# Optimization experiments

Hardware: AMD Instinct MI355X
Metric: run time of the kernel (lower is better)

Reference implementation:

```python
import jax, jax.numpy as jnp
import numpy as np
from jax import lax

BS = 8  # block size
NF = 64  # num_feat

def _dct_mat(n=BS):
    k = np.arange(n)
    D = np.cos(np.pi * (2 * k[None, :] + 1) * k[:, None] / (2 * n)) * np.sqrt(2.0 / n)
    D[0] = np.sqrt(1.0 / n)
    return jnp.asarray(D, dtype=jnp.float32)  # orthonormal DCT-II basis [8,8]

D_DCT = _dct_mat()

def conv2d(x, w, b, stride=1, padding=0, dilation=1, groups=1):
    out = lax.conv_general_dilated(
        x, w, window_strides=(stride, stride),
        padding=[(padding, padding), (padding, padding)],
        rhs_dilation=(dilation, dilation),
        feature_group_count=groups,
        dimension_numbers=('NCHW', 'OIHW', 'NCHW'))
    return out + b[None, :, None, None]

def block_dct_idct(x, bs=BS):
    # fused per-8x8-block DDCT followed by IDDCT (orthonormal basis ->
    # mathematically identity, computed explicitly as in the original loop)
    B, C, H, W = x.shape
    xb = x.reshape(B, C, H // bs, bs, W // bs, bs)
    CB = jnp.einsum('ij,bchjwk,lk->bchiwl', D_DCT, xb, D_DCT)   # D X D^T
    out = jnp.einsum('ji,bchjwk,kl->bchiwl', D_DCT, CB, D_DCT)  # D^T Y D
    return out.reshape(B, C, H, W)

def setup_inputs() -> dict:
    key = jax.random.key(0)
    ks = jax.random.split(key, 16)
    s = 0.05
    inp = {
        'x': jax.random.normal(ks[0], (2, 72, 256, 256), dtype=jnp.float32),
        'conv_w': jax.random.normal(ks[1], (64, 72, 3, 3), dtype=jnp.float32) * s,
        'conv_b': jnp.zeros((64,), dtype=jnp.float32),
        # 7 distinct directional_dct_layer instances (branch 6 reuses layer 4's weights, as in the source)
        'ddct_w': jax.random.normal(ks[2], (7, 64, 64, 3, 3), dtype=jnp.float32) * s,
        'ddct_b': jnp.zeros((7, 64), dtype=jnp.float32),
        'dctc_w': jax.random.normal(ks[3], (7, 64, 1, 3, 3), dtype=jnp.float32) * s,  # groups=64 depthwise
        'dctc_b': jnp.zeros((7, 64), dtype=jnp.float32),
        'dw1_w': jax.random.normal(ks[4], (32, 72, 3, 3), dtype=jnp.float32) * s,
        'dw1_b': jnp.zeros((32,), dtype=jnp.float32),
        'dw3_w': jax.random.normal(ks[5], (512, 32, 1, 1), dtype=jnp.float32) * s,
        'dw3_b': jnp.zeros((512,), dtype=jnp.float32),
        'ar_w': jax.random.normal(ks[6], (72, 512, 3, 3), dtype=jnp.float32) * s,
        'ar_b': jnp.zeros((72,), dtype=jnp.float32),
    }
    return inp

def reference(x, conv_w, conv_b, ddct_w, ddct_b, dctc_w, dctc_b,
              dw1_w, dw1_b, dw3_w, dw3_b, ar_w, ar_b):
    B, _, H, W = x.shape
    feat = jax.nn.gelu(conv2d(x, conv_w, conv_b, padding=1), approximate=False)
    # branches use layers [0,1,3,4,5,6(->4),7,8]; branch 6 reuses conv_dct_4
    layer_idx = [0, 1, 2, 3, 4, 3, 5, 6]
    outs = []
    for li in layer_idx:
        y = jax.nn.gelu(conv2d(feat, ddct_w[li], ddct_b[li], padding=1), approximate=False) + feat
        y = conv2d(y, dctc_w[li], dctc_b[li], stride=8, padding=2, dilation=2, groups=NF)
        y = block_dct_idct(y)
        y = jax.image.resize(y, (B, NF, H, W), method='bilinear')  # align_corners=False
        outs.append(y)
    w = jax.nn.sigmoid(conv2d(jax.nn.relu(conv2d(x, dw1_w, dw1_b, padding=1)), dw3_w, dw3_b, padding=0))
    gated = jnp.concatenate([o * w[:, i * NF:(i + 1) * NF] for i, o in enumerate(outs)], axis=1)
    return conv2d(gated, ar_w, ar_b, padding=1)
```

## Files before the change

kernel.cpp:

```cpp
#include <hip/hip_runtime.h>
#include <hip/hip_bf16.h>

#define BB 2
#define HH 256
#define WW 256
#define HW (HH*WW)
#define GP 258
#define GPP (GP*GP)

typedef __attribute__((ext_vector_type(8))) short bf16x8;
typedef __attribute__((ext_vector_type(4))) float f32x4;

__device__ __forceinline__ float geluf(float x) {
    return 0.5f * x * (1.0f + erff(x * 0.7071067811865475f));
}

__device__ __forceinline__ ushort f2bf(float f) {
    __hip_bfloat16 h = __float2bfloat16(f);
    return *reinterpret_cast<ushort*>(&h);
}
__device__ __forceinline__ float bf2f(ushort u) {
    uint v = ((uint)u) << 16;
    return *reinterpret_cast<float*>(&v);
}

__device__ __forceinline__ int dec96(int i) {
    int q = i / 3, r = i - q * 3;
    return q * 8 + (r == 0 ? 0 : (r == 1 ? 2 : 6));
}

__global__ __launch_bounds__(256) void xpose_kernel(
    const float* __restrict__ x, ushort* __restrict__ xt)
{
    const int pix = blockIdx.x * 256 + threadIdx.x;
    const int b   = pix >> 16;
    const int rem = pix & 65535;

    uint w[48];
    const float* xb = x + (size_t)b * 72 * HW + rem;
    #pragma unroll
    for (int i = 0; i < 36; ++i) {
        const ushort lo = f2bf(xb[(size_t)(2 * i)     * HW]);
        const ushort hi = f2bf(xb[(size_t)(2 * i + 1) * HW]);
        w[i] = (uint)lo | ((uint)hi << 16);
    }
    #pragma unroll
    for (int i = 36; i < 48; ++i) w[i] = 0;

    uint* dst = reinterpret_cast<uint*>(xt + (size_t)pix * 96);
    #pragma unroll
    for (int k = 0; k < 12; ++k) {
        uint4 u = { w[4*k], w[4*k+1], w[4*k+2], w[4*k+3] };
        *reinterpret_cast<uint4*>(dst + 4 * k) = u;
    }
}

__global__ __launch_bounds__(256) void prepack_w1_kernel(
    const float* __restrict__ conv_w, const float* __restrict__ dw1_w,
    ushort* __restrict__ wpc1)
{
    const int idx = blockIdx.x * 256 + threadIdx.x;
    if (idx >= 9 * 3 * 6 * 64) return;
    const int lane = idx & 63;
    int rest = idx >> 6;
    const int mf = rest % 6; rest /= 6;
    const int cb = rest % 3;
    const int t  = rest / 3;
    const int co  = mf * 16 + (lane & 15);
    const int ci0 = cb * 32 + (lane >> 4) * 8;
    ushort* dst = wpc1 + (size_t)idx * 8;
    #pragma unroll
    for (int j = 0; j < 8; ++j) {
        const int ci = ci0 + j;
        float w = 0.0f;
        if (ci < 72)
            w = (co < 64) ? conv_w[((size_t)co * 72 + ci) * 9 + t]
                          : dw1_w[((size_t)(co - 64) * 72 + ci) * 9 + t];
        dst[j] = f2bf(w);
    }
}

__global__ __launch_bounds__(256) void conv1dw1_mfma_kernel(
    const ushort* __restrict__ xt, const ushort* __restrict__ wpc1,
    const float* __restrict__ conv_b, const float* __restrict__ dw1_b,
    ushort* __restrict__ fg, float* __restrict__ relu1)
{
    const int lane = threadIdx.x & 63;
    const int wave = threadIdx.x >> 6;
    const int l15  = lane & 15;
    const int lg   = lane >> 4;

    const int bid  = blockIdx.x;
    const int b    = bid >> 9;
    const int rest = bid & 511;
    const int y    = rest >> 1;
    const int x0   = (rest & 1) * 128 + wave * 32;

    f32x4 acc[6][2];
    #pragma unroll
    for (int mf = 0; mf < 6; ++mf)
        #pragma unroll
        for (int nf = 0; nf < 2; ++nf)
            acc[mf][nf] = (f32x4){0.f, 0.f, 0.f, 0.f};

    const bf16x8 zero8 = {};

    #pragma unroll 1
    for (int t = 0; t < 9; ++t) {
        const int dy = t / 3 - 1, dx = t % 3 - 1;
        const int yy = y + dy;
        if ((unsigned)yy >= (unsigned)HH) continue;

        const int xA = x0 + l15 + dx;
        const int xB = xA + 16;
        const bool va = (unsigned)xA < (unsigned)WW;
        const bool vb = (unsigned)xB < (unsigned)WW;
        const int xAc = min(max(xA, 0), WW - 1);
        const int xBc = min(xB, WW - 1);

        const ushort* rowbase = xt + ((size_t)(b * HH + yy) * WW) * 96;
        const ushort* pA = rowbase + (size_t)xAc * 96 + lg * 8;
        const ushort* pB = rowbase + (size_t)xBc * 96 + lg * 8;
        const ushort* wp = wpc1 + (size_t)(t * 3) * (6 * 512) + lane * 8;

        #pragma unroll
        for (int cb = 0; cb < 3; ++cb) {
            bf16x8 B0 = *reinterpret_cast<const bf16x8*>(pA + cb * 32);
            bf16x8 B1 = *reinterpret_cast<const bf16x8*>(pB + cb * 32);
            B0 = va ? B0 : zero8;
            B1 = vb ? B1 : zero8;
            const ushort* wpc = wp + (size_t)cb * (6 * 512);
            #pragma unroll
            for (int mf = 0; mf < 6; ++mf) {
                const bf16x8 A = *reinterpret_cast<const bf16x8*>(wpc + mf * 512);
                acc[mf][0] = __builtin_amdgcn_mfma_f32_16x16x32_bf16(A, B0, acc[mf][0], 0, 0, 0);
                acc[mf][1] = __builtin_amdgcn_mfma_f32_16x16x32_bf16(A, B1, acc[mf][1], 0, 0, 0);
            }
        }
    }

    #pragma unroll
    for (int nf = 0; nf < 2; ++nf) {
        const int xx = x0 + nf * 16 + l15;
        ushort* fgp = fg + ((size_t)(b * HH + y) * WW + xx) * 64;
        #pragma unroll
        for (int mf = 0; mf < 4; ++mf) {
            const int co = mf * 16 + lg * 4;
            ushort pk[4];
            #pragma unroll
            for (int r = 0; r < 4; ++r)
                pk[r] = f2bf(geluf(acc[mf][nf][r] + conv_b[co + r]));
            *reinterpret_cast<uint2*>(fgp + co) = *reinterpret_cast<uint2*>(pk);
        }
    }
    #pragma unroll
    for (int mf = 4; mf < 6; ++mf) {
        const int co = (mf - 4) * 16 + lg * 4;
        #pragma unroll
        for (int nf = 0; nf < 2; ++nf) {
            const int xx = x0 + nf * 16 + l15;
            float* op = relu1 + ((size_t)(b * 32 + co) * HH + y) * WW + xx;
            #pragma unroll
            for (int r = 0; r < 4; ++r)
                op[(size_t)r * HW] = fmaxf(acc[mf][nf][r] + dw1_b[co + r], 0.0f);
        }
    }
}

__global__ __launch_bounds__(256) void prepack_wb_kernel(
    const float* __restrict__ ddct_w, ushort* __restrict__ wpb)
{
    const int idx = blockIdx.x * 256 + threadIdx.x;
    if (idx >= 7 * 9 * 2 * 4 * 64) return;
    const int lane = idx & 63;
    int rest = idx >> 6;
    const int mf = rest & 3; rest >>= 2;
    const int cb = rest & 1; rest >>= 1;
    const int t  = rest % 9;
    const int li = rest / 9;
    const int co  = mf * 16 + (lane & 15);
    const int ci0 = cb * 32 + (lane >> 4) * 8;
    ushort* dst = wpb + (size_t)idx * 8;
    #pragma unroll
    for (int j = 0; j < 8; ++j)
        dst[j] = f2bf(ddct_w[(((size_t)li * 64 + co) * 64 + ci0 + j) * 9 + t]);
}

__global__ __launch_bounds__(256) void branch_mfma_kernel(
    const ushort* __restrict__ fg, const ushort* __restrict__ wpb,
    const float* __restrict__ ddct_b, float* __restrict__ ycomp)
{
    const int lane = threadIdx.x & 63;
    const int wave = threadIdx.x >> 6;
    const int l15  = lane & 15;
    const int lg   = lane >> 4;

    int bid = blockIdx.x;
    const int t72 = bid % 72; bid /= 72;
    const int b  = bid & 1;
    const int li = bid >> 1;
    const int widx = t72 * 4 + wave;
    const int r  = widx / 3;
    const int c0 = (widx - r * 3) * 32;
    const int R  = dec96(r);

    const int cA = c0 + l15, cB = cA + 16;
    const int CA = dec96(cA), CB2 = dec96(cB);

    f32x4 acc[4][2];
    #pragma unroll
    for (int mf = 0; mf < 4; ++mf)
        #pragma unroll
        for (int nf = 0; nf < 2; ++nf)
            acc[mf][nf] = (f32x4){0.f, 0.f, 0.f, 0.f};

    const bf16x8 zero8 = {};
    const ushort* fgb = fg + (size_t)b * HW * 64;

    #pragma unroll 1
    for (int t = 0; t < 9; ++t) {
        const int dy = t / 3 - 1, dx = t % 3 - 1;
        const int yy = R + dy;
        if ((unsigned)yy >= (unsigned)HH) continue;

        const int xA = CA + dx, xB = CB2 + dx;
        const bool va = (unsigned)xA < (unsigned)WW;
        const bool vb = (unsigned)xB < (unsigned)WW;
        const int xAc = min(max(xA, 0), WW - 1);
        const int xBc = min(max(xB, 0), WW - 1);

        const ushort* rowb = fgb + (size_t)yy * WW * 64;
        const ushort* pA = rowb + (size_t)xAc * 64 + lg * 8;
        const ushort* pB = rowb + (size_t)xBc * 64 + lg * 8;
        const ushort* wp = wpb + (size_t)((li * 9 + t) * 2) * (4 * 512) + lane * 8;

        #pragma unroll
        for (int cb = 0; cb < 2; ++cb) {
            bf16x8 B0 = *reinterpret_cast<const bf16x8*>(pA + cb * 32);
            bf16x8 B1 = *reinterpret_cast<const bf16x8*>(pB + cb * 32);
            B0 = va ? B0 : zero8;
            B1 = vb ? B1 : zero8;
            const ushort* wpc = wp + (size_t)cb * (4 * 512);
            #pragma unroll
            for (int mf = 0; mf < 4; ++mf) {
                const bf16x8 A = *reinterpret_cast<const bf16x8*>(wpc + mf * 512);
                acc[mf][0] = __builtin_amdgcn_mfma_f32_16x16x32_bf16(A, B0, acc[mf][0], 0, 0, 0);
                acc[mf][1] = __builtin_amdgcn_mfma_f32_16x16x32_bf16(A, B1, acc[mf][1], 0, 0, 0);
            }
        }
    }

    #pragma unroll
    for (int nf = 0; nf < 2; ++nf) {
        const int c = c0 + nf * 16 + l15;
        const int C = dec96(c);
        const ushort* res = fgb + ((size_t)R * WW + C) * 64;
        #pragma unroll
        for (int mf = 0; mf < 4; ++mf) {
            const int co = mf * 16 + lg * 4;
            ushort r4[4];
            *reinterpret_cast<uint2*>(r4) = *reinterpret_cast<const uint2*>(res + co);
            #pragma unroll
            for (int rr = 0; rr < 4; ++rr) {
                const float v = geluf(acc[mf][nf][rr] + ddct_b[li * 64 + co + rr]) + bf2f(r4[rr]);
                ycomp[((((size_t)li * BB + b) * 64 + co + rr) * 96 + r) * 96 + c] = v;
            }
        }
    }
}

__global__ __launch_bounds__(256) void dctc_kernel(
    const float* __restrict__ ycomp, const float* __restrict__ dctc_w,
    const float* __restrict__ dctc_b, float* __restrict__ s_all)
{
    const int idx = blockIdx.x * 256 + threadIdx.x;
    if (idx >= 7 * BB * 64 * 32 * 32) return;
    const int ow = idx & 31;
    const int oh = (idx >> 5) & 31;
    const int c  = (idx >> 10) & 63;
    const int b  = (idx >> 16) & (BB - 1);
    const int li = idx >> 17;

    const float* yc = ycomp + (((size_t)li * BB + b) * 64 + c) * (96 * 96);
    const float* w  = dctc_w + (li * 64 + c) * 9;
    float acc = dctc_b[li * 64 + c];
    #pragma unroll
    for (int ky = 0; ky < 3; ++ky) {
        const int cr = 3 * oh + ky - 1;
        if (cr < 0) continue;
        #pragma unroll
        for (int kx = 0; kx < 3; ++kx) {
            const int cc = 3 * ow + kx - 1;
            if (cc < 0) continue;
            acc = fmaf(yc[cr * 96 + cc], w[ky * 3 + kx], acc);
        }
    }
    s_all[idx] = acc;
}

__global__ __launch_bounds__(256) void prepack_w3_kernel(
    const float* __restrict__ dw3_w, float* __restrict__ dw3t)
{
    const int idx = blockIdx.x * 256 + threadIdx.x;
    if (idx >= 32 * 512) return;
    const int ch = idx & 511;
    const int k  = idx >> 9;
    dw3t[k * 512 + ch] = dw3_w[ch * 32 + k];
}

__global__ __launch_bounds__(256) void halo_zero_kernel(ushort* __restrict__ gt)
{
    const int PB = 2 * GP * 64 + 2 * 256 * 64;
    const int i = blockIdx.x * 256 + threadIdx.x;
    if (i >= BB * PB) return;
    const int b = i / PB;
    int r = i - b * PB;
    size_t px;
    int c4;
    if (r < 2 * GP * 64) {
        const int rr = r / (GP * 64);
        int rem = r - rr * (GP * 64);
        const int xp = rem / 64; c4 = rem % 64;
        px = (size_t)(rr ? GP - 1 : 0) * GP + xp;
    } else {
        r -= 2 * GP * 64;
        const int side = r / (256 * 64);
        int rem = r - side * (256 * 64);
        const int yp = 1 + rem / 64; c4 = rem % 64;
        px = (size_t)yp * GP + (side ? GP - 1 : 0);
    }
    const uint4 z = {0u, 0u, 0u, 0u};
    *reinterpret_cast<uint4*>(gt + ((size_t)b * GPP + px) * 512 + c4 * 8) = z;
}

__global__ __launch_bounds__(256, 3) void gated_nhwc_kernel(
    const float* __restrict__ relu1, const float* __restrict__ dw3t,
    const float* __restrict__ dw3_b, const float* __restrict__ s_all,
    ushort* __restrict__ gt)
{
    __shared__ float sm[32][32];
    const int pix0 = blockIdx.x * 32;
    const int b  = pix0 >> 16;
    const int y  = (pix0 >> 8) & 255;
    const int x0 = pix0 & 255;

    {
        const int spx = threadIdx.x & 31;
        const int k0  = threadIdx.x >> 5;
        const float* rbase = relu1 + (size_t)b * 32 * HW + (size_t)y * WW + x0 + spx;
        #pragma unroll
        for (int i = 0; i < 4; ++i)
            sm[k0 + 8 * i][spx] = rbase[(size_t)(k0 + 8 * i) * HW];
    }
    __syncthreads();

    const int ch0 = threadIdx.x * 2;
    const int branch = ch0 >> 6;
    const int c0 = ch0 & 63;
    const int lmap[8] = {0, 1, 2, 3, 4, 3, 5, 6};
    const int li = lmap[branch];

    const float bb0 = dw3_b[ch0], bb1 = dw3_b[ch0 + 1];

    float2 wreg[32];
    #pragma unroll
    for (int k = 0; k < 32; ++k)
        wreg[k] = *reinterpret_cast<const float2*>(dw3t + k * 512 + ch0);

    float acc0[32], acc1[32];
    #pragma unroll
    for (int px = 0; px < 32; ++px) { acc0[px] = bb0; acc1[px] = bb1; }

    #pragma unroll
    for (int k = 0; k < 32; ++k) {
        const float w0k = wreg[k].x;
        const float w1k = wreg[k].y;
        const float4* row = reinterpret_cast<const float4*>(&sm[k][0]);
        #pragma unroll
        for (int q = 0; q < 8; ++q) {
            const float4 r4 = row[q];
            acc0[q*4+0] = fmaf(r4.x, w0k, acc0[q*4+0]);
            acc0[q*4+1] = fmaf(r4.y, w0k, acc0[q*4+1]);
            acc0[q*4+2] = fmaf(r4.z, w0k, acc0[q*4+2]);
            acc0[q*4+3] = fmaf(r4.w, w0k, acc0[q*4+3]);
            acc1[q*4+0] = fmaf(r4.x, w1k, acc1[q*4+0]);
            acc1[q*4+1] = fmaf(r4.y, w1k, acc1[q*4+1]);
            acc1[q*4+2] = fmaf(r4.z, w1k, acc1[q*4+2]);
            acc1[q*4+3] = fmaf(r4.w, w1k, acc1[q*4+3]);
        }
    }

    const float* sp0 = s_all + (((size_t)li * BB + b) * 64 + c0) * 1024;
    const float* sp1 = sp0 + 1024;

    const float sy = (y + 0.5f) * 0.125f - 0.5f;
    const float fy0f = floorf(sy);
    const float fy = sy - fy0f;
    int y0 = (int)fy0f;
    const int y1 = min(y0 + 1, 31);
    y0 = max(y0, 0);

    float n0[6], n1[6];
    const int xb = (x0 >> 3) - 1;
    #pragma unroll
    for (int jj = 0; jj < 6; ++jj) {
        const int xn = min(max(xb + jj, 0), 31);
        const float a00 = sp0[y0 * 32 + xn], a01 = sp0[y1 * 32 + xn];
        const float a10 = sp1[y0 * 32 + xn], a11 = sp1[y1 * 32 + xn];
        n0[jj] = a00 + fy * (a01 - a00);
        n1[jj] = a10 + fy * (a11 - a10);
    }

    ushort* gbase = gt + (((size_t)b * GPP) + (size_t)(y + 1) * GP + (x0 + 1)) * 512 + ch0;
    #pragma unroll
    for (int px = 0; px < 32; ++px) {
        const int   j  = (px + 4) >> 3;
        const float fx = (float)((px + 4) & 7) * 0.125f + 0.0625f;
        const float va = n0[j] + fx * (n0[j + 1] - n0[j]);
        const float vb = n1[j] + fx * (n1[j + 1] - n1[j]);
        const float g0 = 1.0f / (1.0f + exp2f(-1.4426950408889634f * acc0[px]));
        const float g1 = 1.0f / (1.0f + exp2f(-1.4426950408889634f * acc1[px]));
        const uint pack = (uint)f2bf(va * g0) | ((uint)f2bf(vb * g1) << 16);
        *reinterpret_cast<uint*>(gbase + (size_t)px * 512) = pack;
    }
}

__global__ __launch_bounds__(256) void prepack_w_kernel(
    const float* __restrict__ ar_w, ushort* __restrict__ wpack)
{
    const int idx = blockIdx.x * 256 + threadIdx.x;
    if (idx >= 16 * 9 * 5 * 64) return;
    const int lane = idx & 63;
    int rest = idx >> 6;
    const int mf = rest % 5; rest /= 5;
    const int t  = rest % 9;
    const int cb = rest / 9;
    const int co  = mf * 16 + (lane & 15);
    const int ci0 = cb * 32 + (lane >> 4) * 8;
    ushort* dst = wpack + (size_t)idx * 8;
    #pragma unroll
    for (int j = 0; j < 8; ++j) {
        const float w = (co < 72) ? ar_w[((size_t)co * 512 + ci0 + j) * 9 + t] : 0.0f;
        dst[j] = f2bf(w);
    }
}

#define WPK_CHUNK (9 * 5 * 512)

__global__ __launch_bounds__(256, 2) void conv_ar_mfma_kernel(
    const ushort* __restrict__ gt, const ushort* __restrict__ wpack,
    const float* __restrict__ ar_b, float* __restrict__ out)
{
    __shared__ ushort smw[WPK_CHUNK];
    const int tid  = threadIdx.x;
    const int lane = tid & 63;
    const int wave = tid >> 6;
    const int l15  = lane & 15;
    const int lg   = lane >> 4;

    const int lb = (blockIdx.x & 7) * 64 + (blockIdx.x >> 3);
    const int b  = lb >> 8;
    const int y  = lb & 255;
    const int x0 = wave * 64;

    f32x4 acc[5][4];
    #pragma unroll
    for (int mf = 0; mf < 5; ++mf)
        #pragma unroll
        for (int nf = 0; nf < 4; ++nf)
            acc[mf][nf] = (f32x4){0.f, 0.f, 0.f, 0.f};

    const ushort* rowp[3];
    #pragma unroll
    for (int dy = 0; dy < 3; ++dy)
        rowp[dy] = gt + ((size_t)b * GPP + (size_t)(y + dy) * GP) * 512;
    int off[3][4];
    #pragma unroll
    for (int dx = 0; dx < 3; ++dx)
        #pragma unroll
        for (int nf = 0; nf < 4; ++nf)
            off[dx][nf] = (x0 + nf * 16 + l15 + dx) * 512 + lg * 8;

    uint4 streg[12];
    {
        const uint4* s = reinterpret_cast<const uint4*>(wpack);
        #pragma unroll
        for (int i = 0; i < 12; ++i) {
            const int e = i * 256 + tid;
            streg[i] = (e < 2880) ? s[e] : (uint4){0u, 0u, 0u, 0u};
        }
        uint4* d = reinterpret_cast<uint4*>(smw);
        #pragma unroll
        for (int i = 0; i < 12; ++i) {
            const int e = i * 256 + tid;
            if (e < 2880) d[e] = streg[i];
        }
    }
    __syncthreads();

    #pragma unroll 1
    for (int cb = 0; cb < 16; ++cb) {
        if (cb < 15) {
            const uint4* s = reinterpret_cast<const uint4*>(
                wpack + (size_t)(cb + 1) * WPK_CHUNK);
            #pragma unroll
            for (int i = 0; i < 12; ++i) {
                const int e = i * 256 + tid;
                if (e < 2880) streg[i] = s[e];
            }
        }

        const int cbo = cb * 32;
        bf16x8 Bcur[4], Bnxt[4];
        #pragma unroll
        for (int nf = 0; nf < 4; ++nf)
            Bcur[nf] = *reinterpret_cast<const bf16x8*>(rowp[0] + off[0][nf] + cbo);

        #pragma unroll
        for (int t = 0; t < 9; ++t) {
            if (t < 8) {
                const int dyn = (t + 1) / 3, dxn = (t + 1) % 3;
                #pragma unroll
                for (int nf = 0; nf < 4; ++nf)
                    Bnxt[nf] = *reinterpret_cast<const bf16x8*>(
                        rowp[dyn] + off[dxn][nf] + cbo);
            }
            #pragma unroll
            for (int mf = 0; mf < 5; ++mf) {
                const bf16x8 A = *reinterpret_cast<const bf16x8*>(
                    smw + (t * 5 + mf) * 512 + lane * 8);
                #pragma unroll
                for (int nf = 0; nf < 4; ++nf)
                    acc[mf][nf] = __builtin_amdgcn_mfma_f32_16x16x32_bf16(
                        A, Bcur[nf], acc[mf][nf], 0, 0, 0);
            }
            if (t < 8) {
                #pragma unroll
                for (int nf = 0; nf < 4; ++nf) Bcur[nf] = Bnxt[nf];
            }
        }

        __syncthreads();
        if (cb < 15) {
            uint4* d = reinterpret_cast<uint4*>(smw);
            #pragma unroll
            for (int i = 0; i < 12; ++i) {
                const int e = i * 256 + tid;
                if (e < 2880) d[e] = streg[i];
            }
        }
        __syncthreads();
    }

    #pragma unroll
    for (int mf = 0; mf < 5; ++mf) {
        const int co = mf * 16 + lg * 4;
        if (co >= 72) continue;
        #pragma unroll
        for (int nf = 0; nf < 4; ++nf) {
            const int x = x0 + nf * 16 + l15;
            float* op = out + (((size_t)(b * 72 + co) * HH + y) * WW) + x;
            #pragma unroll
            for (int r = 0; r < 4; ++r)
                op[(size_t)r * HW] = acc[mf][nf][r] + ar_b[co + r];
        }
    }
}

extern "C" void kernel_launch(void* const* d_in, const int* in_sizes, int n_in,
                              void* d_out, int out_size, void* d_ws, size_t ws_size,
                              hipStream_t stream) {
    const float* x      = (const float*)d_in[0];
    const float* conv_w = (const float*)d_in[1];
    const float* conv_b = (const float*)d_in[2];
    const float* ddct_w = (const float*)d_in[3];
    const float* ddct_b = (const float*)d_in[4];
    const float* dctc_w = (const float*)d_in[5];
    const float* dctc_b = (const float*)d_in[6];
    const float* dw1_w  = (const float*)d_in[7];
    const float* dw1_b  = (const float*)d_in[8];
    const float* dw3_w  = (const float*)d_in[9];
    const float* dw3_b  = (const float*)d_in[10];
    const float* ar_w   = (const float*)d_in[11];
    const float* ar_b   = (const float*)d_in[12];
    float* out = (float*)d_out;

    float* ws = (float*)d_ws;
    ushort* gated_t = (ushort*)ws;
    ushort* fg    = (ushort*)ws;
    float* ycomp  = ws + 4194304;
    float* s_all  = ws + 34080768;
    float* relu1  = ws + 34998272;
    ushort* wpack = (ushort*)(ws + 39192576);
    ushort* wpb   = (ushort*)(ws + 39376896);
    ushort* wpc1  = (ushort*)(ws + 39505920);
    ushort* xt    = (ushort*)(ws + 39547392);
    float* dw3t   = ws + 45838848;

    prepack_w_kernel<<<dim3(180), dim3(256), 0, stream>>>(ar_w, wpack);
    prepack_wb_kernel<<<dim3(126), dim3(256), 0, stream>>>(ddct_w, wpb);
    prepack_w1_kernel<<<dim3(41), dim3(256), 0, stream>>>(conv_w, dw1_w, wpc1);
    prepack_w3_kernel<<<dim3(64), dim3(256), 0, stream>>>(dw3_w, dw3t);
    xpose_kernel<<<dim3(BB * HW / 256), dim3(256), 0, stream>>>(x, xt);

    conv1dw1_mfma_kernel<<<dim3(BB * HH * 2), dim3(256), 0, stream>>>(
        xt, wpc1, conv_b, dw1_b, fg, relu1);

    branch_mfma_kernel<<<dim3(7 * BB * 72), dim3(256), 0, stream>>>(
        fg, wpb, ddct_b, ycomp);

    dctc_kernel<<<dim3((7 * BB * 64 * 32 * 32) / 256), dim3(256), 0, stream>>>(
        ycomp, dctc_w, dctc_b, s_all);

    halo_zero_kernel<<<dim3(514), dim3(256), 0, stream>>>(gated_t);

    gated_nhwc_kernel<<<dim3(BB * HW / 32), dim3(256), 0, stream>>>(
        relu1, dw3t, dw3_b, s_all, gated_t);

    conv_ar_mfma_kernel<<<dim3(BB * HH), dim3(256), 0, stream>>>(
        gated_t, wpack, ar_b, out);
}
```

Measured before the change: 396.1 us.

## Read AR conv weights directly from global and halve per-wave tile for occupancy

The final 512->72 3x3 conv kernel drops its shared-memory weight staging and barrier-synchronised double buffering. Each lane now loads its MFMA A fragments straight from the prepacked global weight buffer, relying on L1/L2 caching. The per-wave output tile shrinks from 64 to 32 pixels, the grid doubles, and launch bounds rise to 4 blocks per CU to raise occupancy. The B prefetch also now carries across channel blocks. The cost is more global and cache traffic for weights and less weight reuse per load.

```diff
diff --git a/kernel.cpp b/kernel.cpp
--- a/kernel.cpp
+++ b/kernel.cpp
@@ -447,109 +447,75 @@
 
 #define WPK_CHUNK (9 * 5 * 512)
 
-__global__ __launch_bounds__(256, 2) void conv_ar_mfma_kernel(
+__global__ __launch_bounds__(256, 4) void conv_ar_mfma_kernel(
     const ushort* __restrict__ gt, const ushort* __restrict__ wpack,
     const float* __restrict__ ar_b, float* __restrict__ out)
 {
-    __shared__ ushort smw[WPK_CHUNK];
-    const int tid  = threadIdx.x;
-    const int lane = tid & 63;
-    const int wave = tid >> 6;
+    const int lane = threadIdx.x & 63;
+    const int wave = threadIdx.x >> 6;
     const int l15  = lane & 15;
     const int lg   = lane >> 4;
 
-    const int lb = (blockIdx.x & 7) * 64 + (blockIdx.x >> 3);
-    const int b  = lb >> 8;
-    const int y  = lb & 255;
-    const int x0 = wave * 64;
-
-    f32x4 acc[5][4];
+    const int lb = (blockIdx.x & 7) * 128 + (blockIdx.x >> 3);
+    const int b  = lb >> 9;
+    const int y  = (lb >> 1) & 255;
+    const int x0 = (lb & 1) * 128 + wave * 32;
+
+    f32x4 acc[5][2];
     #pragma unroll
     for (int mf = 0; mf < 5; ++mf)
         #pragma unroll
-        for (int nf = 0; nf < 4; ++nf)
+        for (int nf = 0; nf < 2; ++nf)
             acc[mf][nf] = (f32x4){0.f, 0.f, 0.f, 0.f};
 
     const ushort* rowp[3];
     #pragma unroll
     for (int dy = 0; dy < 3; ++dy)
         rowp[dy] = gt + ((size_t)b * GPP + (size_t)(y + dy) * GP) * 512;
-    int off[3][4];
+    int off[3][2];
     #pragma unroll
     for (int dx = 0; dx < 3; ++dx)
         #pragma unroll
-        for (int nf = 0; nf < 4; ++nf)
+        for (int nf = 0; nf < 2; ++nf)
             off[dx][nf] = (x0 + nf * 16 + l15 + dx) * 512 + lg * 8;
 
-    uint4 streg[12];
-    {
-        const uint4* s = reinterpret_cast<const uint4*>(wpack);
-        #pragma unroll
-        for (int i = 0; i < 12; ++i) {
-            const int e = i * 256 + tid;
-            streg[i] = (e < 2880) ? s[e] : (uint4){0u, 0u, 0u, 0u};
-        }
-        uint4* d = reinterpret_cast<uint4*>(smw);
-        #pragma unroll
-        for (int i = 0; i < 12; ++i) {
-            const int e = i * 256 + tid;
-            if (e < 2880) d[e] = streg[i];
-        }
-    }
-    __syncthreads();
+    const ushort* wl = wpack + lane * 8;
+
+    bf16x8 Bcur[2], Bnxt[2];
+    #pragma unroll
+    for (int nf = 0; nf < 2; ++nf)
+        Bcur[nf] = *reinterpret_cast<const bf16x8*>(rowp[0] + off[0][nf]);
 
     #pragma unroll 1
     for (int cb = 0; cb < 16; ++cb) {
-        if (cb < 15) {
-            const uint4* s = reinterpret_cast<const uint4*>(
-                wpack + (size_t)(cb + 1) * WPK_CHUNK);
-            #pragma unroll
-            for (int i = 0; i < 12; ++i) {
-                const int e = i * 256 + tid;
-                if (e < 2880) streg[i] = s[e];
-            }
-        }
-
         const int cbo = cb * 32;
-        bf16x8 Bcur[4], Bnxt[4];
-        #pragma unroll
-        for (int nf = 0; nf < 4; ++nf)
-            Bcur[nf] = *reinterpret_cast<const bf16x8*>(rowp[0] + off[0][nf] + cbo);
-
+        const ushort* wt = wl + (size_t)cb * WPK_CHUNK;
         #pragma unroll
         for (int t = 0; t < 9; ++t) {
             if (t < 8) {
                 const int dyn = (t + 1) / 3, dxn = (t + 1) % 3;
                 #pragma unroll
-                for (int nf = 0; nf < 4; ++nf)
+                for (int nf = 0; nf < 2; ++nf)
                     Bnxt[nf] = *reinterpret_cast<const bf16x8*>(
                         rowp[dyn] + off[dxn][nf] + cbo);
+            } else if (cb < 15) {
+                #pragma unroll
+                for (int nf = 0; nf < 2; ++nf)
+                    Bnxt[nf] = *reinterpret_cast<const bf16x8*>(
+                        rowp[0] + off[0][nf] + cbo + 32);
             }
             #pragma unroll
             for (int mf = 0; mf < 5; ++mf) {
                 const bf16x8 A = *reinterpret_cast<const bf16x8*>(
-                    smw + (t * 5 + mf) * 512 + lane * 8);
+                    wt + (t * 5 + mf) * 512);
                 #pragma unroll
-                for (int nf = 0; nf < 4; ++nf)
+                for (int nf = 0; nf < 2; ++nf)
                     acc[mf][nf] = __builtin_amdgcn_mfma_f32_16x16x32_bf16(
                         A, Bcur[nf], acc[mf][nf], 0, 0, 0);
             }
-            if (t < 8) {
-                #pragma unroll
-                for (int nf = 0; nf < 4; ++nf) Bcur[nf] = Bnxt[nf];
-            }
-        }
-
-        __syncthreads();
-        if (cb < 15) {
-            uint4* d = reinterpret_cast<uint4*>(smw);
-            #pragma unroll
-            for (int i = 0; i < 12; ++i) {
-                const int e = i * 256 + tid;
-                if (e < 2880) d[e] = streg[i];
-            }
-        }
-        __syncthreads();
+            #pragma unroll
+            for (int nf = 0; nf < 2; ++nf) Bcur[nf] = Bnxt[nf];
+        }
     }
 
     #pragma unroll
@@ -557,7 +523,7 @@
         const int co = mf * 16 + lg * 4;
         if (co >= 72) continue;
         #pragma unroll
-        for (int nf = 0; nf < 4; ++nf) {
+        for (int nf = 0; nf < 2; ++nf) {
             const int x = x0 + nf * 16 + l15;
             float* op = out + (((size_t)(b * 72 + co) * HH + y) * WW) + x;
             #pragma unroll
@@ -617,6 +583,6 @@
     gated_nhwc_kernel<<<dim3(BB * HW / 32), dim3(256), 0, stream>>>(
         relu1, dw3t, dw3_b, s_all, gated_t);
 
-    conv_ar_mfma_kernel<<<dim3(BB * HH), dim3(256), 0, stream>>>(
+    conv_ar_mfma_kernel<<<dim3(BB * HH * 2), dim3(256), 0, stream>>>(
         gated_t, wpack, ar_b, out);
 }
```

Measured after the change: 461.8 us. 1.17x slower.
